# Optimization experiments

Hardware: AMD Instinct MI355X
Metric: run time of the kernel (lower is better)

## Reference

```python
import jax, jax.numpy as jnp
import numpy as np

EMBED_DIM = 2048
NUM_HEADS = 16
HEAD_DIM = EMBED_DIM // NUM_HEADS
BASE = 10000.0


def rotate_half(x):
    half = x.shape[-1] // 2
    x1, x2 = x[..., :half], x[..., half:]
    return jnp.concatenate([-x2, x1], axis=-1)


def apply_rope(x, base=BASE):
    # x: [B, H, S, Dh]
    S, Dh = x.shape[-2], x.shape[-1]
    inv_freq = 1.0 / (base ** (jnp.arange(0, Dh, 2, dtype=jnp.float32) / Dh))
    t = jnp.arange(S, dtype=jnp.float32)
    freqs = jnp.einsum('i,j->ij', t, inv_freq)          # [S, Dh/2]
    emb = jnp.concatenate([freqs, freqs], axis=-1)      # [S, Dh]
    return x * jnp.cos(emb) + rotate_half(x) * jnp.sin(emb)


def setup_inputs() -> dict:
    key = jax.random.key(0)
    ks = jax.random.split(key, 9)
    B, S, D = 2, 2048, EMBED_DIM
    xavier = lambda k, shape: jax.random.uniform(
        k, shape, jnp.float32, -1.0, 1.0) * float(np.sqrt(6.0 / (shape[0] + shape[1])))
    return {
        'x': jax.random.normal(ks[0], (B, S, D), jnp.float32),
        'q_w': xavier(ks[1], (D, D)),
        'k_w': xavier(ks[2], (D, D)),
        'v_w': xavier(ks[3], (D, D)),
        'q_b': jnp.zeros((D,), jnp.float32),
        'k_b': jnp.zeros((D,), jnp.float32),
        'v_b': jnp.zeros((D,), jnp.float32),
        'out_w': xavier(ks[4], (D, D)),
        'out_b': jnp.zeros((D,), jnp.float32),
    }


def reference(x, q_w, k_w, v_w, q_b, k_b, v_b, out_w, out_b):
    B, S, D = x.shape
    H, Dh = NUM_HEADS, HEAD_DIM
    scaling = Dh ** -0.5
    # F.linear(x, W, b) = x @ W.T + b
    q = (x @ q_w.T + q_b).reshape(B, S, H, Dh).transpose(0, 2, 1, 3)
    k = (x @ k_w.T + k_b).reshape(B, S, H, Dh).transpose(0, 2, 1, 3)
    v = (x @ v_w.T + v_b).reshape(B, S, H, Dh).transpose(0, 2, 1, 3)
    q = apply_rope(q)
    k = apply_rope(k)
    attn = jnp.einsum('bhqd,bhkd->bhqk', q, k) * scaling
    probs = jax.nn.softmax(attn, axis=-1)
    out = jnp.einsum('bhqk,bhkd->bhqd', probs, v)
    out = out.transpose(0, 2, 1, 3).reshape(B, S, D)
    return out @ out_w.T + out_b
```

## Files before the change

kernel.cpp:

```cpp
#include <hip/hip_runtime.h>
#include <stdint.h>

typedef __bf16 bf16;
typedef __bf16 bf16x4 __attribute__((ext_vector_type(4)));
typedef __bf16 bf16x8 __attribute__((ext_vector_type(8)));
typedef float f32x4 __attribute__((ext_vector_type(4)));

#define DM 2048
#define MM 4096
#define MFMA16(a, b, c) __builtin_amdgcn_mfma_f32_16x16x32_bf16(a, b, c, 0, 0, 0)

__device__ __forceinline__ void gload_lds16(const void* g, void* l) {
  __builtin_amdgcn_global_load_lds((const __attribute__((address_space(1))) uint32_t*)g,
                                   (__attribute__((address_space(3))) uint32_t*)l, 16, 0, 0);
}

__global__ __launch_bounds__(256) void cvt_f32_bf16(
    const float* __restrict__ s0, const float* __restrict__ s1,
    const float* __restrict__ s2, const float* __restrict__ s3,
    const float* __restrict__ s4,
    bf16* __restrict__ d0, bf16* __restrict__ d1, bf16* __restrict__ d2,
    bf16* __restrict__ d3, bf16* __restrict__ d4)
{
  const size_t i4 = (size_t)(blockIdx.x * 256 + threadIdx.x) * 4;
  const float* s; bf16* d; size_t off;
  if      (i4 <  8388608u) { s = s0; d = d0; off = i4;             }
  else if (i4 < 12582912u) { s = s1; d = d1; off = i4 -  8388608u; }
  else if (i4 < 16777216u) { s = s2; d = d2; off = i4 - 12582912u; }
  else if (i4 < 20971520u) { s = s3; d = d3; off = i4 - 16777216u; }
  else                     { s = s4; d = d4; off = i4 - 20971520u; }
  const float4 v = *(const float4*)(s + off);
  bf16x4 o = { (bf16)v.x, (bf16)v.y, (bf16)v.z, (bf16)v.w };
  *(bf16x4*)(d + off) = o;
}

__global__ __launch_bounds__(256, 2) void gemm_qkv_fused(
    const bf16* __restrict__ A,
    const bf16* __restrict__ Wq, const bf16* __restrict__ Wk, const bf16* __restrict__ Wv,
    const float* __restrict__ qb, const float* __restrict__ kb, const float* __restrict__ vb,
    bf16* __restrict__ Cq, bf16* __restrict__ Ck, bf16* __restrict__ Cv)
{
  __shared__ __align__(16) bf16 smem[32768];
  bf16* As = smem;
  bf16* Ws = smem + 8192;

  const int id = blockIdx.x;
  const int xcd = id & 7, jj = id >> 3;
  const int n0 = (xcd * 2 + (jj >> 5)) * 128;
  const int m0 = (jj & 31) * 128;

  const int t = threadIdx.x;
  const int wave = t >> 6, lane = t & 63;
  const int quad = lane >> 4, c16 = lane & 15;
  const int wr = wave >> 1, wc = wave & 1;

  f32x4 acc[3][4][4] = {};

  const int srow = t >> 3;
  const int scol = ((t & 7) ^ (srow & 7)) * 8;
  const bf16* gA  = A  + (size_t)(m0 + srow) * DM + scol;
  const bf16* gW0 = Wq + (size_t)(n0 + srow) * DM + scol;
  const bf16* gW1 = Wk + (size_t)(n0 + srow) * DM + scol;
  const bf16* gW2 = Wv + (size_t)(n0 + srow) * DM + scol;

  for (int k0 = 0; k0 < DM; k0 += 64) {
#pragma unroll
    for (int rr = 0; rr < 4; ++rr) {
      const size_t go = (size_t)(rr * 32) * DM;
      const int lo = (rr * 256 + wave * 64) * 8;
      gload_lds16(gA  + go, As + lo);
      gload_lds16(gW0 + go, Ws + lo);
      gload_lds16(gW1 + go, Ws + 8192 + lo);
      gload_lds16(gW2 + go, Ws + 16384 + lo);
    }
    gA += 64; gW0 += 64; gW1 += 64; gW2 += 64;
    __syncthreads();

#pragma unroll
    for (int ks = 0; ks < 2; ++ks) {
      bf16x8 af[4];
#pragma unroll
      for (int i = 0; i < 4; ++i) {
        const int row = wr * 64 + i * 16 + c16;
        const int gi = (ks * 4 + quad) ^ (row & 7);
        af[i] = *(const bf16x8*)&As[row * 64 + gi * 8];
      }
#pragma unroll
      for (int z = 0; z < 3; ++z) {
        bf16x8 bfr[4];
#pragma unroll
        for (int jx = 0; jx < 4; ++jx) {
          const int row = wc * 64 + jx * 16 + c16;
          const int gi = (ks * 4 + quad) ^ (row & 7);
          bfr[jx] = *(const bf16x8*)&Ws[z * 8192 + row * 64 + gi * 8];
        }
#pragma unroll
        for (int i = 0; i < 4; ++i)
#pragma unroll
          for (int jx = 0; jx < 4; ++jx)
            acc[z][i][jx] = MFMA16(af[i], bfr[jx], acc[z][i][jx]);
      }
    }
    __syncthreads();
  }

  const int h = n0 >> 7;
#pragma unroll
  for (int jx = 0; jx < 4; ++jx) {
    const int d = wc * 64 + jx * 16 + c16;
    const float bv = vb[n0 + d];
#pragma unroll
    for (int i = 0; i < 4; ++i) {
      const int row = m0 + wr * 64 + i * 16 + quad * 4;
      const int b = row >> 11, s = row & 2047;
      bf16x4 o;
#pragma unroll
      for (int r = 0; r < 4; ++r) o[r] = (bf16)(acc[2][i][jx][r] + bv);
      *(bf16x4*)&Cv[((size_t)((b * 16 + h) * 128 + d)) * 2048 + s] = o;
    }
  }

  bf16* Tl = smem;
#pragma unroll
  for (int z = 0; z < 2; ++z) {
    __syncthreads();
#pragma unroll
    for (int jx = 0; jx < 4; ++jx) {
      const int col = wc * 64 + jx * 16 + c16;
      const float bv = (z == 0 ? qb : kb)[n0 + col];
#pragma unroll
      for (int i = 0; i < 4; ++i) {
        const int row = wr * 64 + i * 16 + quad * 4;
#pragma unroll
        for (int r = 0; r < 4; ++r)
          Tl[(row + r) * 136 + col] = (bf16)(acc[z][i][jx][r] + bv);
      }
    }
    __syncthreads();
    bf16* C = (z == 0) ? Cq : Ck;
    const float scale = (z == 0) ? 0.08838834764831845f * 1.4426950408889634f : 1.0f;
#pragma unroll
    for (int rr = 0; rr < 4; ++rr) {
      const int row = rr * 32 + (t >> 3);
      const int d0 = (t & 7) * 8;
      const int s = (m0 + row) & 2047;
      bf16x8 xa = *(const bf16x8*)&Tl[row * 136 + d0];
      bf16x8 xb = *(const bf16x8*)&Tl[row * 136 + d0 + 64];
      bf16x8 o1, o2;
#pragma unroll
      for (int j = 0; j < 8; ++j) {
        const float inv_freq = __expf((float)(d0 + j) * -0.14391156514261228f);
        float sn, cs;
        __sincosf((float)s * inv_freq, &sn, &cs);
        const float a = (float)xa[j], bb = (float)xb[j];
        o1[j] = (bf16)((a * cs - bb * sn) * scale);
        o2[j] = (bf16)((bb * cs + a * sn) * scale);
      }
      *(bf16x8*)&C[(size_t)(m0 + row) * DM + n0 + d0]      = o1;
      *(bf16x8*)&C[(size_t)(m0 + row) * DM + n0 + d0 + 64] = o2;
    }
  }
}

__global__ __launch_bounds__(256, 2) void gemm_bias_f32(
    const bf16* __restrict__ A, const bf16* __restrict__ W,
    const float* __restrict__ bias, float* __restrict__ C)
{
  __shared__ __align__(16) bf16 As[8192];
  __shared__ __align__(16) bf16 Bs[8192];
  const int id = blockIdx.x;
  const int xcd = id & 7, jj = id >> 3;
  const int n0 = (xcd * 2 + (jj >> 5)) * 128;
  const int m0 = (jj & 31) * 128;

  const int t = threadIdx.x;
  const int wave = t >> 6, lane = t & 63;
  const int quad = lane >> 4, c16 = lane & 15;
  const int wr = wave >> 1, wc = wave & 1;

  f32x4 acc[4][4] = {};
  const int srow = t >> 3;
  const int scol = ((t & 7) ^ (srow & 7)) * 8;
  const bf16* gA = A + (size_t)(m0 + srow) * DM + scol;
  const bf16* gB = W + (size_t)(n0 + srow) * DM + scol;

  for (int k0 = 0; k0 < DM; k0 += 64) {
#pragma unroll
    for (int rr = 0; rr < 4; ++rr) {
      const size_t go = (size_t)(rr * 32) * DM;
      const int lo = (rr * 256 + wave * 64) * 8;
      gload_lds16(gA + go, As + lo);
      gload_lds16(gB + go, Bs + lo);
    }
    gA += 64; gB += 64;
    __syncthreads();

#pragma unroll
    for (int ks = 0; ks < 2; ++ks) {
      bf16x8 af[4], bfr[4];
#pragma unroll
      for (int i = 0; i < 4; ++i) {
        const int row = wr * 64 + i * 16 + c16;
        const int gi = (ks * 4 + quad) ^ (row & 7);
        af[i] = *(const bf16x8*)&As[row * 64 + gi * 8];
      }
#pragma unroll
      for (int jx = 0; jx < 4; ++jx) {
        const int row = wc * 64 + jx * 16 + c16;
        const int gi = (ks * 4 + quad) ^ (row & 7);
        bfr[jx] = *(const bf16x8*)&Bs[row * 64 + gi * 8];
      }
#pragma unroll
      for (int i = 0; i < 4; ++i)
#pragma unroll
        for (int jx = 0; jx < 4; ++jx)
          acc[i][jx] = MFMA16(af[i], bfr[jx], acc[i][jx]);
    }
    __syncthreads();
  }

#pragma unroll
  for (int jx = 0; jx < 4; ++jx) {
    const int col = n0 + wc * 64 + jx * 16 + c16;
    const float bv = bias[col];
#pragma unroll
    for (int i = 0; i < 4; ++i) {
      const int row = m0 + wr * 64 + i * 16 + quad * 4;
#pragma unroll
      for (int r = 0; r < 4; ++r)
        C[(size_t)(row + r) * DM + col] = acc[i][jx][r] + bv;
    }
  }
}

__global__ __launch_bounds__(256, 3) void attn(
    const bf16* __restrict__ Q, const bf16* __restrict__ K,
    const bf16* __restrict__ Vt, bf16* __restrict__ O)
{
  __shared__ __align__(16) bf16 Ks[4][64][32];
  __shared__ __align__(16) bf16 Vs[2][128][32];
  __shared__ __align__(16) bf16 Ps[4][2][16][80];
  const int t = threadIdx.x;
  const int wave = t >> 6, lane = t & 63;
  const int quad = lane >> 4, c16 = lane & 15;
  const int id = blockIdx.x;
  const int xcd = id & 7, jj = id >> 3;
  const int bh = xcd * 4 + (jj >> 4);
  const int q0 = (jj & 15) * 128;
  const int b = bh >> 4, h = bh & 15;

  bf16x8 qf[2][4];
#pragma unroll
  for (int g = 0; g < 2; ++g) {
    const bf16* qrow = Q + (size_t)(b * 2048 + q0 + wave * 32 + g * 16 + c16) * 2048
                         + (size_t)h * 128 + quad * 8;
#pragma unroll
    for (int ks = 0; ks < 4; ++ks) qf[g][ks] = *(const bf16x8*)(qrow + ks * 32);
  }

  float l_i[2] = {0.f, 0.f};
  f32x4 o_acc[2][8] = {};

  const bf16* Kg = K + (size_t)(b * 2048) * 2048 + (size_t)h * 128;
  const bf16* Vg = Vt + (size_t)bh * 128 * 2048;

  for (int kt = 0; kt < 32; ++kt) {
    const int kt0 = kt * 64;
#pragma unroll
    for (int rr = 0; rr < 4; ++rr) {
      const int s = rr * 256 + t;
      const int ks = s >> 8, krow = (s >> 2) & 63, c8 = s & 3;
      gload_lds16(Kg + (size_t)(kt0 + krow) * 2048 + ks * 32 + c8 * 8,
                  (bf16*)Ks + (size_t)(rr * 256 + wave * 64) * 8);
    }
#pragma unroll
    for (int rr = 0; rr < 4; ++rr) {
      const int s = rr * 256 + t;
      const int kc = s >> 9, d = (s >> 2) & 127, c8 = s & 3;
      gload_lds16(Vg + (size_t)d * 2048 + kt0 + kc * 32 + c8 * 8,
                  (bf16*)Vs + (size_t)(rr * 256 + wave * 64) * 8);
    }
    __syncthreads();

    f32x4 st[2][4] = {};
#pragma unroll
    for (int ks = 0; ks < 4; ++ks)
#pragma unroll
      for (int nt = 0; nt < 4; ++nt) {
        bf16x8 kf = *(const bf16x8*)&Ks[ks][nt * 16 + c16][quad * 8];
        st[0][nt] = MFMA16(kf, qf[0][ks], st[0][nt]);
        st[1][nt] = MFMA16(kf, qf[1][ks], st[1][nt]);
      }

#pragma unroll
    for (int g = 0; g < 2; ++g) {
      float ps = 0.f;
#pragma unroll
      for (int nt = 0; nt < 4; ++nt) {
        bf16x4 pk;
#pragma unroll
        for (int r = 0; r < 4; ++r) {
          const float p = exp2f(st[g][nt][r]);
          ps += p;
          pk[r] = (bf16)p;
        }
        *(bf16x4*)&Ps[wave][g][c16][nt * 16 + quad * 4] = pk;
      }
      l_i[g] += ps;
    }

#pragma unroll
    for (int kc = 0; kc < 2; ++kc) {
      bf16x8 pf0 = *(const bf16x8*)&Ps[wave][0][c16][kc * 32 + quad * 8];
      bf16x8 pf1 = *(const bf16x8*)&Ps[wave][1][c16][kc * 32 + quad * 8];
#pragma unroll
      for (int dt = 0; dt < 8; ++dt) {
        bf16x8 vf = *(const bf16x8*)&Vs[kc][dt * 16 + c16][quad * 8];
        o_acc[0][dt] = MFMA16(vf, pf0, o_acc[0][dt]);
        o_acc[1][dt] = MFMA16(vf, pf1, o_acc[1][dt]);
      }
    }
    __syncthreads();
  }

#pragma unroll
  for (int g = 0; g < 2; ++g) {
    float l = l_i[g];
    l += __shfl_xor(l, 16, 64);
    l += __shfl_xor(l, 32, 64);
    const float invl = 1.0f / l;
    const int qrow = q0 + wave * 32 + g * 16 + c16;
    bf16* orow = O + (size_t)(b * 2048 + qrow) * 2048 + (size_t)h * 128 + quad * 4;
#pragma unroll
    for (int dt = 0; dt < 8; ++dt) {
      bf16x4 o;
#pragma unroll
      for (int r = 0; r < 4; ++r) o[r] = (bf16)(o_acc[g][dt][r] * invl);
      *(bf16x4*)(orow + dt * 16) = o;
    }
  }
}

extern "C" void kernel_launch(void* const* d_in, const int* in_sizes, int n_in,
                              void* d_out, int out_size, void* d_ws, size_t ws_size,
                              hipStream_t stream)
{
  (void)in_sizes; (void)n_in; (void)out_size; (void)ws_size;
  const float* x   = (const float*)d_in[0];
  const float* q_w = (const float*)d_in[1];
  const float* k_w = (const float*)d_in[2];
  const float* v_w = (const float*)d_in[3];
  const float* q_b = (const float*)d_in[4];
  const float* k_b = (const float*)d_in[5];
  const float* v_b = (const float*)d_in[6];
  const float* o_w = (const float*)d_in[7];
  const float* o_b = (const float*)d_in[8];

  const size_t NELEM = (size_t)MM * DM;
  const size_t WELEM = (size_t)DM * DM;
  bf16* Xb  = (bf16*)d_ws;
  bf16* Wq  = Xb + NELEM;
  bf16* Wk  = Wq + WELEM;
  bf16* Wv  = Wk + WELEM;
  bf16* Wo  = Wv + WELEM;
  bf16* Q   = Wo + WELEM;
  bf16* Kb  = Q  + NELEM;
  bf16* Vt  = Kb + NELEM;
  bf16* attnO = Xb;

  cvt_f32_bf16<<<24576, 256, 0, stream>>>(x, q_w, k_w, v_w, o_w, Xb, Wq, Wk, Wv, Wo);

  gemm_qkv_fused<<<512, 256, 0, stream>>>(Xb, Wq, Wk, Wv, q_b, k_b, v_b, Q, Kb, Vt);
  attn<<<512, 256, 0, stream>>>(Q, Kb, Vt, attnO);
  gemm_bias_f32<<<512, 256, 0, stream>>>(attnO, Wo, o_b, (float*)d_out);
}
```

Baseline: 391.9 us.

## Double-buffer K/V tiles with XOR-swizzled LDS layout in attention kernel

The attention loop now works on 32-key tiles held in two LDS buffers, loading the next tile while the current one is computed, so only one barrier per iteration is needed. K and V tiles are stored with an XOR swizzle on the 8-element chunk index to reduce LDS bank conflicts on the fragment reads. The smaller tile halves the per-iteration score and P buffers. Launch bounds drop from 3 to 2 waves-per-SIMD occupancy, giving the compiler more registers at the cost of fewer resident blocks, and the doubled iteration count adds loop overhead.

Result: faster. 369.6 us (-5.7%).

```diff
diff --git a/kernel.cpp b/kernel.cpp
--- a/kernel.cpp
+++ b/kernel.cpp
@@ -233,13 +233,13 @@
   }
 }
 
-__global__ __launch_bounds__(256, 3) void attn(
+__global__ __launch_bounds__(256, 2) void attn(
     const bf16* __restrict__ Q, const bf16* __restrict__ K,
     const bf16* __restrict__ Vt, bf16* __restrict__ O)
 {
-  __shared__ __align__(16) bf16 Ks[4][64][32];
+  __shared__ __align__(16) bf16 Ks[2][4][32][32];
   __shared__ __align__(16) bf16 Vs[2][128][32];
-  __shared__ __align__(16) bf16 Ps[4][2][16][80];
+  __shared__ __align__(16) bf16 Ps[4][2][16][40];
   const int t = threadIdx.x;
   const int wave = t >> 6, lane = t & 63;
   const int quad = lane >> 4, c16 = lane & 15;
@@ -264,30 +264,38 @@
   const bf16* Kg = K + (size_t)(b * 2048) * 2048 + (size_t)h * 128;
   const bf16* Vg = Vt + (size_t)bh * 128 * 2048;
 
-  for (int kt = 0; kt < 32; ++kt) {
-    const int kt0 = kt * 64;
-#pragma unroll
-    for (int rr = 0; rr < 4; ++rr) {
-      const int s = rr * 256 + t;
-      const int ks = s >> 8, krow = (s >> 2) & 63, c8 = s & 3;
-      gload_lds16(Kg + (size_t)(kt0 + krow) * 2048 + ks * 32 + c8 * 8,
-                  (bf16*)Ks + (size_t)(rr * 256 + wave * 64) * 8);
-    }
-#pragma unroll
-    for (int rr = 0; rr < 4; ++rr) {
-      const int s = rr * 256 + t;
-      const int kc = s >> 9, d = (s >> 2) & 127, c8 = s & 3;
-      gload_lds16(Vg + (size_t)d * 2048 + kt0 + kc * 32 + c8 * 8,
-                  (bf16*)Vs + (size_t)(rr * 256 + wave * 64) * 8);
-    }
-    __syncthreads();
-
-    f32x4 st[2][4] = {};
+  auto stage = [&](int kt0, int nb) {
+#pragma unroll
+    for (int rr = 0; rr < 2; ++rr) {
+      const int g = rr * 256 + t;
+      const int ks = g >> 7, krow = (g >> 2) & 31, c8 = g & 3;
+      gload_lds16(Kg + (size_t)(kt0 + krow) * 2048 + ks * 32 + ((c8 ^ ((krow >> 1) & 3)) * 8),
+                  (bf16*)Ks[nb] + (rr * 256 + wave * 64) * 8);
+    }
+#pragma unroll
+    for (int rr = 0; rr < 2; ++rr) {
+      const int g = rr * 256 + t;
+      const int d = g >> 2, c8 = g & 3;
+      gload_lds16(Vg + (size_t)d * 2048 + kt0 + ((c8 ^ ((d >> 1) & 3)) * 8),
+                  (bf16*)Vs[nb] + (rr * 256 + wave * 64) * 8);
+    }
+  };
+
+  stage(0, 0);
+  __syncthreads();
+
+#pragma unroll 2
+  for (int kt = 0; kt < 64; ++kt) {
+    const int cb = kt & 1;
+    if (kt < 63) stage((kt + 1) * 32, cb ^ 1);
+
+    f32x4 st[2][2] = {};
 #pragma unroll
     for (int ks = 0; ks < 4; ++ks)
 #pragma unroll
-      for (int nt = 0; nt < 4; ++nt) {
-        bf16x8 kf = *(const bf16x8*)&Ks[ks][nt * 16 + c16][quad * 8];
+      for (int nt = 0; nt < 2; ++nt) {
+        const int row = nt * 16 + c16;
+        bf16x8 kf = *(const bf16x8*)&Ks[cb][ks][row][(quad ^ ((row >> 1) & 3)) * 8];
         st[0][nt] = MFMA16(kf, qf[0][ks], st[0][nt]);
         st[1][nt] = MFMA16(kf, qf[1][ks], st[1][nt]);
       }
@@ -296,7 +304,7 @@
     for (int g = 0; g < 2; ++g) {
       float ps = 0.f;
 #pragma unroll
-      for (int nt = 0; nt < 4; ++nt) {
+      for (int nt = 0; nt < 2; ++nt) {
         bf16x4 pk;
 #pragma unroll
         for (int r = 0; r < 4; ++r) {
@@ -309,17 +317,16 @@
       l_i[g] += ps;
     }
 
-#pragma unroll
-    for (int kc = 0; kc < 2; ++kc) {
-      bf16x8 pf0 = *(const bf16x8*)&Ps[wave][0][c16][kc * 32 + quad * 8];
-      bf16x8 pf1 = *(const bf16x8*)&Ps[wave][1][c16][kc * 32 + quad * 8];
-#pragma unroll
-      for (int dt = 0; dt < 8; ++dt) {
-        bf16x8 vf = *(const bf16x8*)&Vs[kc][dt * 16 + c16][quad * 8];
-        o_acc[0][dt] = MFMA16(vf, pf0, o_acc[0][dt]);
-        o_acc[1][dt] = MFMA16(vf, pf1, o_acc[1][dt]);
-      }
-    }
+    bf16x8 pf0 = *(const bf16x8*)&Ps[wave][0][c16][quad * 8];
+    bf16x8 pf1 = *(const bf16x8*)&Ps[wave][1][c16][quad * 8];
+#pragma unroll
+    for (int dt = 0; dt < 8; ++dt) {
+      const int row = dt * 16 + c16;
+      bf16x8 vf = *(const bf16x8*)&Vs[cb][row][(quad ^ ((row >> 1) & 3)) * 8];
+      o_acc[0][dt] = MFMA16(vf, pf0, o_acc[0][dt]);
+      o_acc[1][dt] = MFMA16(vf, pf1, o_acc[1][dt]);
+    }
+
     __syncthreads();
   }
 
```
